# Kernel optimization log

Measured on AMD Instinct MI355X. Metric: run time of the kernel, lower is better.

The kernel has to match this reference:

```python
import jax, jax.numpy as jnp
import numpy as np

B, CY, CS, D, H, W = 4, 256, 256, 256, 64, 64


def pe2d(C, H, W, dtype=jnp.float32):
    """PositionalEncodingPermute2D: returns [C, H, W]. Assumes ch_half even (C=256 -> 128)."""
    ch_half = (C + 1) // 2
    inv = 1.0 / (10000.0 ** (jnp.arange(0, ch_half, 2, dtype=jnp.float32) / ch_half))  # [ch_half//2]
    tH = jnp.arange(H, dtype=jnp.float32)
    tW = jnp.arange(W, dtype=jnp.float32)
    sH = tH[:, None] * inv[None, :]                      # [H, ch_half//2]
    sW = tW[:, None] * inv[None, :]                      # [W, ch_half//2]
    embH = jnp.concatenate([jnp.sin(sH), jnp.cos(sH)], -1)  # [H, ch_half]
    embW = jnp.concatenate([jnp.sin(sW), jnp.cos(sW)], -1)  # [W, ch_half]
    E = jnp.zeros((H, W, 2 * ch_half), dtype=dtype)
    E = E.at[:, :, :ch_half].set(jnp.broadcast_to(embW[None, :, :], (H, W, ch_half)).astype(dtype))
    E = E.at[:, :, ch_half:2 * ch_half].set(jnp.broadcast_to(embH[:, None, :], (H, W, ch_half)).astype(dtype))
    return jnp.transpose(E[..., :C], (2, 0, 1))          # [C, H, W]


def conv1x1(x, w, b):
    # x: [B,Cin,H,W], w: [Cout,Cin], b: [Cout]
    return jnp.einsum('bchw,dc->bdhw', x, w) + b[None, :, None, None]


def setup_inputs() -> dict:
    key = jax.random.key(0)
    ks = jax.random.split(key, 12)
    s_in = 1.0 / np.sqrt(D)
    return {
        'Y': jax.random.normal(ks[0], (B, CY, H, W), jnp.float32),
        'S': jax.random.normal(ks[1], (B, CS, H, W), jnp.float32),
        'Wq': jax.random.normal(ks[2], (D, CY), jnp.float32) * s_in,
        'bq': jax.random.normal(ks[3], (D,), jnp.float32) * 0.01,
        'Wk': jax.random.normal(ks[4], (D, CS), jnp.float32) * s_in,
        'bk': jax.random.normal(ks[5], (D,), jnp.float32) * 0.01,
        'Wv': jax.random.normal(ks[6], (D, CS), jnp.float32) * s_in,
        'bv': jax.random.normal(ks[7], (D,), jnp.float32) * 0.01,
        'Wo': jax.random.normal(ks[8], (CS, D), jnp.float32) * s_in,
        'bo': jax.random.normal(ks[9], (CS,), jnp.float32) * 0.01,
    }


def reference(Y, S, Wq, bq, Wk, bk, Wv, bv, Wo, bo):
    b, _, h, w = Y.shape
    d = Wq.shape[0]
    scale = d ** (-0.5)
    Q = conv1x1(Y, Wq, bq)
    K = conv1x1(S, Wk, bk)
    V = conv1x1(S, Wv, bv)
    pe = pe2d(d, h, w, Q.dtype)[None]                    # [1,d,H,W]
    Q = Q + pe
    K = K + pe
    # flatten spatial -> [B, N, d]
    Qf = Q.reshape(b, d, h * w).transpose(0, 2, 1)
    Kf = K.reshape(b, d, h * w).transpose(0, 2, 1)
    Vf = V.reshape(b, d, h * w).transpose(0, 2, 1)
    A = jax.nn.softmax(jnp.einsum('bnd,bmd->bnm', Qf, Kf) * scale, axis=-1)
    Z = jnp.einsum('bnm,bmd->bnd', A, Vf)                # [B,N,d]
    Z = Z.transpose(0, 2, 1).reshape(b, d, h, w)
    return conv1x1(Z, Wo, bo)
```

## Files before the change

kernel.cpp:

```cpp
#include <hip/hip_runtime.h>
#include <stdint.h>


#define NB 4
#define CC 256
#define DD 256
#define NN 4096
#define PS (NB * NN * DD)

typedef float f32x4 __attribute__((ext_vector_type(4)));
typedef unsigned int u32x4 __attribute__((ext_vector_type(4)));
typedef unsigned int u32x2 __attribute__((ext_vector_type(2)));
typedef _Float16 f16x8 __attribute__((ext_vector_type(8)));
typedef __fp16 fp16x2 __attribute__((ext_vector_type(2)));

#define MFMAH(a, b, c) __builtin_amdgcn_mfma_f32_16x16x32_f16((a), (b), (c), 0, 0, 0)

__device__ __forceinline__ uint16_t h2u(_Float16 h) {
    return __builtin_bit_cast(unsigned short, h);
}
__device__ __forceinline__ uint32_t packh(_Float16 a, _Float16 b) {
    return (uint32_t)h2u(a) | ((uint32_t)h2u(b) << 16);
}
__device__ __forceinline__ f16x8 ldsh8(const void* p) {
    return __builtin_bit_cast(f16x8, *(const u32x4*)p);
}
__device__ __forceinline__ void split8h(const float* v, f16x8& hi, f16x8& lo) {
#pragma unroll
    for (int j = 0; j < 8; ++j) {
        _Float16 h = (_Float16)v[j];
        hi[j] = h;
        lo[j] = (_Float16)(v[j] - (float)h);
    }
}

__global__ __launch_bounds__(256) void proj_kernel(
    const float* __restrict__ Y, const float* __restrict__ S,
    const float* __restrict__ Wq, const float* __restrict__ bq,
    const float* __restrict__ Wk, const float* __restrict__ bk,
    const float* __restrict__ Wv, const float* __restrict__ bv,
    uint16_t* __restrict__ Qp, uint16_t* __restrict__ Kp,
    uint16_t* __restrict__ Vp) {
    __shared__ char XsH[64 * 64];
    __shared__ char XsL[64 * 64];
    __shared__ float Bz[64 * 68];

    int bi = blockIdx.x;
    int proj = bi >> 10;
    int rem = bi & 1023;
    int b = rem >> 8;
    int dt = (rem >> 6) & 3;
    int nt = rem & 63;
    int d0 = dt * 64, n0 = nt * 64;

    int t = threadIdx.x;
    int lane = t & 63, wv = t >> 6;
    int g = lane >> 4, li = lane & 15;

    const float* X = (proj == 0 ? Y : S) + (size_t)b * CC * NN;
    const float* W = proj == 0 ? Wq : (proj == 1 ? Wk : Wv);
    const float* bias = proj == 0 ? bq : (proj == 1 ? bk : bv);

    f32x4 acc[4];
#pragma unroll
    for (int i = 0; i < 4; ++i) acc[i] = (f32x4){0.f, 0.f, 0.f, 0.f};

    int nloc = t & 63;
    int cq = t >> 6;
    uint32_t spch = (uint32_t)(cq ^ ((nloc >> 1) & 3));
    uint32_t rpch = (uint32_t)(g ^ ((li >> 1) & 3));

    for (int kk = 0; kk < 8; ++kk) {
        int c0 = kk * 32;
        {
            const float* xp = X + (size_t)(c0 + cq * 8) * NN + n0 + nloc;
            float xv[8];
#pragma unroll
            for (int j = 0; j < 8; ++j) xv[j] = xp[(size_t)j * NN];
            u32x4 hw, lw;
#pragma unroll
            for (int w = 0; w < 4; ++w) {
                float x = xv[2 * w], y = xv[2 * w + 1];
                _Float16 hx = (_Float16)x, hy = (_Float16)y;
                hw[w] = packh(hx, hy);
                lw[w] = packh((_Float16)(x - (float)hx), (_Float16)(y - (float)hy));
            }
            *(u32x4*)(XsH + nloc * 64 + spch * 16) = hw;
            *(u32x4*)(XsL + nloc * 64 + spch * 16) = lw;
        }
        __syncthreads();
        const float* wr = W + (size_t)(d0 + wv * 16 + li) * CC + c0 + g * 8;
        float wvv[8];
        *(float4*)&wvv[0] = ((const float4*)wr)[0];
        *(float4*)&wvv[4] = ((const float4*)wr)[1];
        f16x8 wh, wl;
        split8h(wvv, wh, wl);
#pragma unroll
        for (int nf = 0; nf < 4; ++nf) {
            const char* bp = XsH + (nf * 16 + li) * 64 + rpch * 16;
            f16x8 xh = ldsh8(bp);
            f16x8 xl = ldsh8(XsL + (nf * 16 + li) * 64 + rpch * 16);
            acc[nf] = MFMAH(wh, xh, acc[nf]);
            acc[nf] = MFMAH(wh, xl, acc[nf]);
            acc[nf] = MFMAH(wl, xh, acc[nf]);
        }
        __syncthreads();
    }

    if (proj == 2) {
#pragma unroll
        for (int r = 0; r < 4; ++r) {
            int d = d0 + wv * 16 + g * 4 + r;
            float bs = bias[d];
#pragma unroll
            for (int nf = 0; nf < 4; ++nf) {
                int n = n0 + nf * 16 + li;
                float v = acc[nf][r] + bs;
                Vp[(size_t)(b * DD + d) * NN + n] = h2u((_Float16)v);
            }
        }
    } else {
        const float QSCALE = 0.0625f * 1.4426950408889634f;
#pragma unroll
        for (int r = 0; r < 4; ++r) {
            int d = d0 + wv * 16 + g * 4 + r;
            float bs = bias[d];
            int jj = d & 63;
            float inv = exp2f((float)jj * -0.20762050593046f);
#pragma unroll
            for (int nf = 0; nf < 4; ++nf) {
                int n = n0 + nf * 16 + li;
                float v = acc[nf][r] + bs;
                float pos = (d < 128) ? (float)(n & 63) : (float)(n >> 6);
                float ar = pos * inv;
                v += (d & 64) ? cosf(ar) : sinf(ar);
                if (proj == 0) v *= QSCALE;
                Bz[(nf * 16 + li) * 68 + wv * 16 + g * 4 + r] = v;
            }
        }
        __syncthreads();
        {
            int nl = t >> 2;
            int dk = (t & 3) * 16;
            float vv[16];
#pragma unroll
            for (int q = 0; q < 4; ++q)
                *(float4*)&vv[q * 4] = *(const float4*)&Bz[nl * 68 + dk + q * 4];
            u32x4 w0, w1;
#pragma unroll
            for (int w = 0; w < 4; ++w)
                w0[w] = packh((_Float16)vv[2 * w], (_Float16)vv[2 * w + 1]);
#pragma unroll
            for (int w = 0; w < 4; ++w)
                w1[w] = packh((_Float16)vv[8 + 2 * w], (_Float16)vv[9 + 2 * w]);
            uint16_t* Ph = (proj == 0) ? Qp : Kp;
            size_t o = (size_t)(b * NN + n0 + nl) * DD + d0 + dk;
            ((u32x4*)(Ph + o))[0] = w0;
            ((u32x4*)(Ph + o))[1] = w1;
        }
    }
}

__global__ __launch_bounds__(256, 1) void attn_kernel(
    const uint16_t* __restrict__ Qp, const uint16_t* __restrict__ Kp,
    const uint16_t* __restrict__ Vp,
    const float* __restrict__ Wo, const float* __restrict__ bo,
    float* __restrict__ Out) {
    extern __shared__ char smem[];

    int t = threadIdx.x;
    int lane = t & 63, wv = t >> 6;
    int g = lane >> 4, li = lane & 15;

    int orig = ((blockIdx.x & 7) << 5) + (blockIdx.x >> 3);
    int b = orig >> 6;
    int nt = orig & 63;
    int n0 = nt * 64;

    f16x8 qh[8];
    {
        size_t qrow = (size_t)(b * NN + n0 + wv * 16 + li) * DD;
#pragma unroll
        for (int kf = 0; kf < 8; ++kf)
            qh[kf] =
                __builtin_bit_cast(f16x8, *(const u32x4*)(Qp + qrow + kf * 32 + g * 8));
    }

    const uint16_t* splane;
    uint32_t dstbase, adv;
    uint32_t soff[16];
    if (wv < 2) {
        splane = Kp + (size_t)b * NN * DD;
        dstbase = (uint32_t)wv * 16384u;
        adv = 64 * 256;
#pragma unroll
        for (int i = 0; i < 16; ++i) {
            int rr = wv * 32 + 2 * i + (lane >> 5);
            int cc = lane & 31;
            soff[i] = (uint32_t)(rr * 256 + ((cc ^ (rr & 7)) * 8));
        }
    } else {
        splane = Vp + (size_t)b * DD * NN;
        dstbase = 65536u + (uint32_t)(wv - 2) * 16384u;
        adv = 64;
#pragma unroll
        for (int i = 0; i < 16; ++i) {
            int rr = (wv - 2) * 128 + i * 8 + (lane >> 3);
            int cc = lane & 7;
            soff[i] = (uint32_t)rr * 4096u + (uint32_t)((cc ^ (rr & 7)) * 8);
        }
    }

    uint32_t PB = 131072u + (uint32_t)wv * 2048u;
    uint32_t ka[8];
#pragma unroll
    for (int kf = 0; kf < 8; ++kf)
        ka[kf] = (uint32_t)li * 512u + (uint32_t)(((kf * 4 + g) ^ (li & 7)) * 16);
    uint32_t va0 = 65536u + (uint32_t)li * 128u + (uint32_t)(((g) ^ (li & 7)) * 16);
    uint32_t va1 = 65536u + (uint32_t)li * 128u + (uint32_t)(((4 + g) ^ (li & 7)) * 16);
    uint32_t pw[4];
#pragma unroll
    for (int mf = 0; mf < 4; ++mf)
        pw[mf] = PB + (uint32_t)li * 128u +
                 (uint32_t)((((2 * mf + (g >> 1))) ^ (li & 7)) * 16) +
                 (uint32_t)((g & 1) * 8);
    uint32_t pr0 = PB + (uint32_t)li * 128u + (uint32_t)(((g) ^ (li & 7)) * 16);
    uint32_t pr1 = PB + (uint32_t)li * 128u + (uint32_t)(((4 + g) ^ (li & 7)) * 16);

    f32x4 acc[16];
#pragma unroll
    for (int i = 0; i < 16; ++i) acc[i] = (f32x4){0.f, 0.f, 0.f, 0.f};
    float mrun = -__builtin_inff();
    float lrun = 0.f;
    f32x4 stA[4], stB[4];

#define STAGEX(tt)                                                                      \
    do {                                                                                \
        uint32_t mo = (uint32_t)(tt)*adv;                                               \
        char* db = smem + (uint32_t)(((tt)&1) * 32768u) + dstbase;                      \
        _Pragma("unroll") for (int i = 0; i < 16; ++i) {                                \
            __builtin_amdgcn_global_load_lds(                                           \
                (const __attribute__((address_space(1))) unsigned int*)(splane +        \
                                                                        soff[i] + mo),  \
                (__attribute__((address_space(3))) unsigned int*)(db + i * 1024), 16, 0,\
                0);                                                                     \
        }                                                                               \
    } while (0)

#define QKPART(T, SC)                                                                   \
    {                                                                                   \
        _Pragma("unroll") for (int mf = 0; mf < 4; ++mf) SC[mf] =                       \
            (f32x4){0.f, 0.f, 0.f, 0.f};                                                \
        __builtin_amdgcn_s_setprio(1);                                                  \
        _Pragma("unroll") for (int kf = 0; kf < 8; ++kf) {                              \
            _Pragma("unroll") for (int mf = 0; mf < 4; ++mf) {                          \
                f16x8 kfr = ldsh8(smem + ka[kf] +                                       \
                                  (uint32_t)(((T)&1) * 32768u + mf * 8192u));           \
                SC[mf] = MFMAH(kfr, qh[kf], SC[mf]);                                    \
            }                                                                           \
        }                                                                               \
        __builtin_amdgcn_s_setprio(0);                                                  \
    }

#define SMPV(T, SP)                                                                     \
    {                                                                                   \
        float sv[16];                                                                   \
        _Pragma("unroll") for (int mf = 0; mf < 4; ++mf)                                \
            _Pragma("unroll") for (int r = 0; r < 4; ++r) sv[mf * 4 + r] = SP[mf][r];   \
        float pm = sv[0];                                                               \
        _Pragma("unroll") for (int j = 1; j < 16; ++j) pm = fmaxf(pm, sv[j]);           \
        pm = fmaxf(pm, __shfl_xor(pm, 16));                                             \
        pm = fmaxf(pm, __shfl_xor(pm, 32));                                             \
        if (__any(pm > mrun + 5.77f)) {                                                 \
            float mnew = fmaxf(mrun, pm);                                               \
            float fac = exp2f(mrun - mnew);                                             \
            lrun *= fac;                                                                \
            _Pragma("unroll") for (int i2 = 0; i2 < 16; ++i2) {                         \
                acc[i2][0] *= fac; acc[i2][1] *= fac;                                   \
                acc[i2][2] *= fac; acc[i2][3] *= fac;                                   \
            }                                                                           \
            mrun = mnew;                                                                \
        }                                                                               \
        float p[16];                                                                    \
        float ps = 0.f;                                                                 \
        _Pragma("unroll") for (int j = 0; j < 16; ++j) {                                \
            p[j] = exp2f(sv[j] - mrun);                                                 \
            ps += p[j];                                                                 \
        }                                                                               \
        uint32_t hw[8];                                                                 \
        _Pragma("unroll") for (int w = 0; w < 8; ++w) hw[w] = __builtin_bit_cast(       \
            uint32_t, __builtin_amdgcn_cvt_pkrtz(p[2 * w], p[2 * w + 1]));              \
        _Pragma("unroll") for (int mf = 0; mf < 4; ++mf) {                              \
            *(u32x2*)(smem + pw[mf]) = (u32x2){hw[2 * mf], hw[2 * mf + 1]};             \
        }                                                                               \
        ps += __shfl_xor(ps, 16);                                                       \
        ps += __shfl_xor(ps, 32);                                                       \
        lrun += ps;                                                                     \
        f16x8 pbh0 = ldsh8(smem + pr0);                                                 \
        f16x8 pbh1 = ldsh8(smem + pr1);                                                 \
        __builtin_amdgcn_s_setprio(1);                                                  \
        _Pragma("unroll") for (int df = 0; df < 16; ++df) {                             \
            uint32_t vo = (uint32_t)((((T)&1) ? 0u : 32768u) + df * 2048u);             \
            f16x8 v0 = ldsh8(smem + va0 + vo);                                          \
            f16x8 v1 = ldsh8(smem + va1 + vo);                                          \
            acc[df] = MFMAH(v0, pbh0, acc[df]);                                         \
            acc[df] = MFMAH(v1, pbh1, acc[df]);                                         \
        }                                                                               \
        __builtin_amdgcn_s_setprio(0);                                                  \
    }

#define ITER(T, SC, SP, DOSM, VMC)                                                      \
    {                                                                                   \
        asm volatile("s_waitcnt vmcnt(" #VMC ")" ::: "memory");                         \
        __builtin_amdgcn_s_barrier();                                                   \
        QKPART(T, SC);                                                                  \
        if (DOSM) SMPV(T, SP);                                                          \
        asm volatile("s_waitcnt lgkmcnt(0)" ::: "memory");                              \
        __builtin_amdgcn_s_barrier();                                                   \
        if (((T) < 62) && (wv < 2)) STAGEX((T) + 2);                                    \
        if (((T) < 63) && (wv >= 2)) STAGEX((T) + 1);                                   \
    }

    if (wv < 2) {
        STAGEX(0);
        STAGEX(1);
    } else {
        STAGEX(0);
    }

    ITER(0, stA, stB, 0, 16);
#pragma unroll 1
    for (int tp = 0; tp < 31; ++tp) {
        ITER(2 * tp + 1, stB, stA, 1, 16);
        ITER(2 * tp + 2, stA, stB, 1, 16);
    }
    ITER(63, stB, stA, 1, 0);
    SMPV(64, stB);

#undef ITER
#undef SMPV
#undef QKPART
#undef STAGEX

    float rl = 1.0f / lrun;
    char* zh = smem;
    char* zl = smem + 32768;
    {
        int n = wv * 16 + li;
#pragma unroll
        for (int df = 0; df < 16; ++df) {
#pragma unroll
            for (int rp = 0; rp < 2; ++rp) {
                float a0 = acc[df][2 * rp] * rl, a1 = acc[df][2 * rp + 1] * rl;
                _Float16 h0 = (_Float16)a0, h1 = (_Float16)a1;
                uint32_t whi = packh(h0, h1);
                uint32_t wlo =
                    packh((_Float16)(a0 - (float)h0), (_Float16)(a1 - (float)h1));
                uint32_t chunk = (uint32_t)((df * 2 + (g >> 1)) ^ (li & 7));
                uint32_t off = (uint32_t)n * 512 + chunk * 16 + (g & 1) * 8 + rp * 4;
                *(uint32_t*)(zh + off) = whi;
                *(uint32_t*)(zl + off) = wlo;
            }
        }
    }
    __syncthreads();

    f32x4 oc[4][4];
#pragma unroll
    for (int i = 0; i < 4; ++i)
#pragma unroll
        for (int j = 0; j < 4; ++j) oc[i][j] = (f32x4){0.f, 0.f, 0.f, 0.f};
    int cs0 = wv * 64;
#pragma unroll 1
    for (int kf = 0; kf < 8; ++kf) {
        f16x8 zhv[4], zlv[4];
#pragma unroll
        for (int nf = 0; nf < 4; ++nf) {
            uint32_t off = (uint32_t)(nf * 16 + li) * 512 +
                           (uint32_t)((kf * 4 + g) ^ (li & 7)) * 16;
            zhv[nf] = ldsh8(zh + off);
            zlv[nf] = ldsh8(zl + off);
        }
#pragma unroll
        for (int csf = 0; csf < 4; ++csf) {
            const float* wr = Wo + (size_t)(cs0 + csf * 16 + li) * DD + kf * 32 + g * 8;
            float wvv[8];
            *(float4*)&wvv[0] = ((const float4*)wr)[0];
            *(float4*)&wvv[4] = ((const float4*)wr)[1];
            f16x8 wh, wl;
            split8h(wvv, wh, wl);
#pragma unroll
            for (int nf = 0; nf < 4; ++nf) {
                oc[csf][nf] = MFMAH(wh, zhv[nf], oc[csf][nf]);
                oc[csf][nf] = MFMAH(wh, zlv[nf], oc[csf][nf]);
                oc[csf][nf] = MFMAH(wl, zhv[nf], oc[csf][nf]);
            }
        }
    }
#pragma unroll
    for (int csf = 0; csf < 4; ++csf) {
#pragma unroll
        for (int r = 0; r < 4; ++r) {
            int cs = cs0 + csf * 16 + g * 4 + r;
            float bb = bo[cs];
#pragma unroll
            for (int nf = 0; nf < 4; ++nf)
                Out[(size_t)(b * 256 + cs) * NN + n0 + nf * 16 + li] =
                    oc[csf][nf][r] + bb;
        }
    }
}

extern "C" void kernel_launch(void* const* d_in, const int* in_sizes, int n_in,
                              void* d_out, int out_size, void* d_ws, size_t ws_size,
                              hipStream_t stream) {
    (void)in_sizes; (void)n_in; (void)out_size; (void)ws_size;
    const float* Y = (const float*)d_in[0];
    const float* S = (const float*)d_in[1];
    const float* Wq = (const float*)d_in[2];
    const float* bq = (const float*)d_in[3];
    const float* Wk = (const float*)d_in[4];
    const float* bk = (const float*)d_in[5];
    const float* Wv = (const float*)d_in[6];
    const float* bv = (const float*)d_in[7];
    const float* Wo = (const float*)d_in[8];
    const float* bo = (const float*)d_in[9];
    float* Out = (float*)d_out;

    uint16_t* ws = (uint16_t*)d_ws;
    uint16_t* Qp = ws + 0 * (size_t)PS;
    uint16_t* Kp = ws + 1 * (size_t)PS;
    uint16_t* Vp = ws + 2 * (size_t)PS;

    (void)hipFuncSetAttribute((const void*)attn_kernel,
                              hipFuncAttributeMaxDynamicSharedMemorySize, 139264);

    proj_kernel<<<3072, 256, 0, stream>>>(Y, S, Wq, bq, Wk, bk, Wv, bv, Qp, Kp, Vp);
    attn_kernel<<<256, 256, 139264, stream>>>(Qp, Kp, Vp, Wo, bo, Out);
}
```

Baseline: 302.8 us.

## Split each key tile across two wave groups and merge softmax partials

```diff
diff --git a/kernel.cpp b/kernel.cpp
--- a/kernel.cpp
+++ b/kernel.cpp
@@ -161,7 +161,7 @@
     }
 }
 
-__global__ __launch_bounds__(256, 1) void attn_kernel(
+__global__ __launch_bounds__(512, 2) void attn_kernel(
     const uint16_t* __restrict__ Qp, const uint16_t* __restrict__ Kp,
     const uint16_t* __restrict__ Vp,
     const float* __restrict__ Wo, const float* __restrict__ bo,
@@ -171,6 +171,7 @@
     int t = threadIdx.x;
     int lane = t & 63, wv = t >> 6;
     int g = lane >> 4, li = lane & 15;
+    int qf = wv & 3, h = wv >> 2;
 
     int orig = ((blockIdx.x & 7) << 5) + (blockIdx.x >> 3);
     int b = orig >> 6;
@@ -179,7 +180,7 @@
 
     f16x8 qh[8];
     {
-        size_t qrow = (size_t)(b * NN + n0 + wv * 16 + li) * DD;
+        size_t qrow = (size_t)(b * NN + n0 + qf * 16 + li) * DD;
 #pragma unroll
         for (int kf = 0; kf < 8; ++kf)
             qh[kf] =
@@ -188,24 +189,24 @@
 
     const uint16_t* splane;
     uint32_t dstbase, adv;
-    uint32_t soff[16];
-    if (wv < 2) {
+    uint32_t soff[8];
+    if (wv < 4) {
         splane = Kp + (size_t)b * NN * DD;
-        dstbase = (uint32_t)wv * 16384u;
+        dstbase = (uint32_t)wv * 8192u;
         adv = 64 * 256;
 #pragma unroll
-        for (int i = 0; i < 16; ++i) {
-            int rr = wv * 32 + 2 * i + (lane >> 5);
+        for (int i = 0; i < 8; ++i) {
+            int rr = wv * 16 + 2 * i + (lane >> 5);
             int cc = lane & 31;
             soff[i] = (uint32_t)(rr * 256 + ((cc ^ (rr & 7)) * 8));
         }
     } else {
         splane = Vp + (size_t)b * DD * NN;
-        dstbase = 65536u + (uint32_t)(wv - 2) * 16384u;
+        dstbase = 65536u + (uint32_t)(wv - 4) * 8192u;
         adv = 64;
 #pragma unroll
-        for (int i = 0; i < 16; ++i) {
-            int rr = (wv - 2) * 128 + i * 8 + (lane >> 3);
+        for (int i = 0; i < 8; ++i) {
+            int rr = (wv - 4) * 64 + i * 8 + (lane >> 3);
             int cc = lane & 7;
             soff[i] = (uint32_t)rr * 4096u + (uint32_t)((cc ^ (rr & 7)) * 8);
         }
@@ -215,30 +216,30 @@
     uint32_t ka[8];
 #pragma unroll
     for (int kf = 0; kf < 8; ++kf)
-        ka[kf] = (uint32_t)li * 512u + (uint32_t)(((kf * 4 + g) ^ (li & 7)) * 16);
-    uint32_t va0 = 65536u + (uint32_t)li * 128u + (uint32_t)(((g) ^ (li & 7)) * 16);
-    uint32_t va1 = 65536u + (uint32_t)li * 128u + (uint32_t)(((4 + g) ^ (li & 7)) * 16);
-    uint32_t pw[4];
-#pragma unroll
-    for (int mf = 0; mf < 4; ++mf)
+        ka[kf] = (uint32_t)(h * 32 + li) * 512u +
+                 (uint32_t)(((kf * 4 + g) ^ (li & 7)) * 16);
+    uint32_t va = 65536u + (uint32_t)li * 128u +
+                  (uint32_t)(((h * 4 + g) ^ (li & 7)) * 16);
+    uint32_t pw[2];
+#pragma unroll
+    for (int mf = 0; mf < 2; ++mf)
         pw[mf] = PB + (uint32_t)li * 128u +
-                 (uint32_t)((((2 * mf + (g >> 1))) ^ (li & 7)) * 16) +
+                 (uint32_t)((((mf * 2 + (g >> 1))) ^ (li & 7)) * 16) +
                  (uint32_t)((g & 1) * 8);
-    uint32_t pr0 = PB + (uint32_t)li * 128u + (uint32_t)(((g) ^ (li & 7)) * 16);
-    uint32_t pr1 = PB + (uint32_t)li * 128u + (uint32_t)(((4 + g) ^ (li & 7)) * 16);
+    uint32_t pr = PB + (uint32_t)li * 128u + (uint32_t)((g ^ (li & 7)) * 16);
 
     f32x4 acc[16];
 #pragma unroll
     for (int i = 0; i < 16; ++i) acc[i] = (f32x4){0.f, 0.f, 0.f, 0.f};
     float mrun = -__builtin_inff();
     float lrun = 0.f;
-    f32x4 stA[4], stB[4];
+    f32x4 stA[2], stB[2];
 
 #define STAGEX(tt)                                                                      \
     do {                                                                                \
         uint32_t mo = (uint32_t)(tt)*adv;                                               \
         char* db = smem + (uint32_t)(((tt)&1) * 32768u) + dstbase;                      \
-        _Pragma("unroll") for (int i = 0; i < 16; ++i) {                                \
+        _Pragma("unroll") for (int i = 0; i < 8; ++i) {                                 \
             __builtin_amdgcn_global_load_lds(                                           \
                 (const __attribute__((address_space(1))) unsigned int*)(splane +        \
                                                                         soff[i] + mo),  \
@@ -249,11 +250,11 @@
 
 #define QKPART(T, SC)                                                                   \
     {                                                                                   \
-        _Pragma("unroll") for (int mf = 0; mf < 4; ++mf) SC[mf] =                       \
+        _Pragma("unroll") for (int mf = 0; mf < 2; ++mf) SC[mf] =                       \
             (f32x4){0.f, 0.f, 0.f, 0.f};                                                \
         __builtin_amdgcn_s_setprio(1);                                                  \
         _Pragma("unroll") for (int kf = 0; kf < 8; ++kf) {                              \
-            _Pragma("unroll") for (int mf = 0; mf < 4; ++mf) {                          \
+            _Pragma("unroll") for (int mf = 0; mf < 2; ++mf) {                          \
                 f16x8 kfr = ldsh8(smem + ka[kf] +                                       \
                                   (uint32_t)(((T)&1) * 32768u + mf * 8192u));           \
                 SC[mf] = MFMAH(kfr, qh[kf], SC[mf]);                                    \
@@ -264,11 +265,11 @@
 
 #define SMPV(T, SP)                                                                     \
     {                                                                                   \
-        float sv[16];                                                                   \
-        _Pragma("unroll") for (int mf = 0; mf < 4; ++mf)                                \
+        float sv[8];                                                                    \
+        _Pragma("unroll") for (int mf = 0; mf < 2; ++mf)                                \
             _Pragma("unroll") for (int r = 0; r < 4; ++r) sv[mf * 4 + r] = SP[mf][r];   \
         float pm = sv[0];                                                               \
-        _Pragma("unroll") for (int j = 1; j < 16; ++j) pm = fmaxf(pm, sv[j]);           \
+        _Pragma("unroll") for (int j = 1; j < 8; ++j) pm = fmaxf(pm, sv[j]);            \
         pm = fmaxf(pm, __shfl_xor(pm, 16));                                             \
         pm = fmaxf(pm, __shfl_xor(pm, 32));                                             \
         if (__any(pm > mrun + 5.77f)) {                                                 \
@@ -281,30 +282,27 @@
             }                                                                           \
             mrun = mnew;                                                                \
         }                                                                               \
-        float p[16];                                                                    \
+        float p[8];                                                                     \
         float ps = 0.f;                                                                 \
-        _Pragma("unroll") for (int j = 0; j < 16; ++j) {                                \
+        _Pragma("unroll") for (int j = 0; j < 8; ++j) {                                 \
             p[j] = exp2f(sv[j] - mrun);                                                 \
             ps += p[j];                                                                 \
         }                                                                               \
-        uint32_t hw[8];                                                                 \
-        _Pragma("unroll") for (int w = 0; w < 8; ++w) hw[w] = __builtin_bit_cast(       \
+        uint32_t hw[4];                                                                 \
+        _Pragma("unroll") for (int w = 0; w < 4; ++w) hw[w] = __builtin_bit_cast(       \
             uint32_t, __builtin_amdgcn_cvt_pkrtz(p[2 * w], p[2 * w + 1]));              \
-        _Pragma("unroll") for (int mf = 0; mf < 4; ++mf) {                              \
+        _Pragma("unroll") for (int mf = 0; mf < 2; ++mf) {                              \
             *(u32x2*)(smem + pw[mf]) = (u32x2){hw[2 * mf], hw[2 * mf + 1]};             \
         }                                                                               \
         ps += __shfl_xor(ps, 16);                                                       \
         ps += __shfl_xor(ps, 32);                                                       \
         lrun += ps;                                                                     \
-        f16x8 pbh0 = ldsh8(smem + pr0);                                                 \
-        f16x8 pbh1 = ldsh8(smem + pr1);                                                 \
+        f16x8 pb = ldsh8(smem + pr);                                                    \
         __builtin_amdgcn_s_setprio(1);                                                  \
         _Pragma("unroll") for (int df = 0; df < 16; ++df) {                             \
             uint32_t vo = (uint32_t)((((T)&1) ? 0u : 32768u) + df * 2048u);             \
-            f16x8 v0 = ldsh8(smem + va0 + vo);                                          \
-            f16x8 v1 = ldsh8(smem + va1 + vo);                                          \
-            acc[df] = MFMAH(v0, pbh0, acc[df]);                                         \
-            acc[df] = MFMAH(v1, pbh1, acc[df]);                                         \
+            f16x8 v0 = ldsh8(smem + va + vo);                                           \
+            acc[df] = MFMAH(v0, pb, acc[df]);                                           \
         }                                                                               \
         __builtin_amdgcn_s_setprio(0);                                                  \
     }
@@ -317,22 +315,22 @@
         if (DOSM) SMPV(T, SP);                                                          \
         asm volatile("s_waitcnt lgkmcnt(0)" ::: "memory");                              \
         __builtin_amdgcn_s_barrier();                                                   \
-        if (((T) < 62) && (wv < 2)) STAGEX((T) + 2);                                    \
-        if (((T) < 63) && (wv >= 2)) STAGEX((T) + 1);                                   \
-    }
-
-    if (wv < 2) {
+        if (((T) < 62) && (wv < 4)) STAGEX((T) + 2);                                    \
+        if (((T) < 63) && (wv >= 4)) STAGEX((T) + 1);                                   \
+    }
+
+    if (wv < 4) {
         STAGEX(0);
         STAGEX(1);
     } else {
         STAGEX(0);
     }
 
-    ITER(0, stA, stB, 0, 16);
+    ITER(0, stA, stB, 0, 8);
 #pragma unroll 1
     for (int tp = 0; tp < 31; ++tp) {
-        ITER(2 * tp + 1, stB, stA, 1, 16);
-        ITER(2 * tp + 2, stA, stB, 1, 16);
+        ITER(2 * tp + 1, stB, stA, 1, 8);
+        ITER(2 * tp + 2, stA, stB, 1, 8);
     }
     ITER(63, stB, stA, 1, 0);
     SMPV(64, stB);
@@ -342,11 +340,41 @@
 #undef QKPART
 #undef STAGEX
 
-    float rl = 1.0f / lrun;
-    char* zh = smem;
-    char* zl = smem + 32768;
-    {
-        int n = wv * 16 + li;
+    __syncthreads();
+    if (wv >= 4) {
+        uint32_t wb = 65536u + (uint32_t)(wv - 4) * 16384u;
+#pragma unroll
+        for (int df = 0; df < 16; ++df)
+            *(f32x4*)(smem + wb + (uint32_t)df * 1024u + (uint32_t)lane * 16u) =
+                acc[df];
+        *(float*)(smem + 147456u + (uint32_t)(wv - 4) * 512u + (uint32_t)lane * 8u) =
+            mrun;
+        *(float*)(smem + 147456u + (uint32_t)(wv - 4) * 512u + (uint32_t)lane * 8u +
+                  4u) = lrun;
+    }
+    __syncthreads();
+
+    if (wv < 4) {
+        float m2 =
+            *(const float*)(smem + 147456u + (uint32_t)wv * 512u + (uint32_t)lane * 8u);
+        float l2 = *(const float*)(smem + 147456u + (uint32_t)wv * 512u +
+                                   (uint32_t)lane * 8u + 4u);
+        float mN = fmaxf(mrun, m2);
+        float f1 = exp2f(mrun - mN);
+        float f2 = exp2f(m2 - mN);
+        float lm = lrun * f1 + l2 * f2;
+        uint32_t wb = 65536u + (uint32_t)wv * 16384u;
+#pragma unroll
+        for (int df = 0; df < 16; ++df) {
+            f32x4 a2 =
+                *(const f32x4*)(smem + wb + (uint32_t)df * 1024u + (uint32_t)lane * 16u);
+#pragma unroll
+            for (int r = 0; r < 4; ++r) acc[df][r] = acc[df][r] * f1 + a2[r] * f2;
+        }
+        float rl = 1.0f / lm;
+        char* zh = smem;
+        char* zl = smem + 32768;
+        int n = qf * 16 + li;
 #pragma unroll
         for (int df = 0; df < 16; ++df) {
 #pragma unroll
@@ -365,12 +393,14 @@
     }
     __syncthreads();
 
-    f32x4 oc[4][4];
-#pragma unroll
-    for (int i = 0; i < 4; ++i)
+    const char* zh = smem;
+    const char* zl = smem + 32768;
+    f32x4 oc[2][4];
+#pragma unroll
+    for (int i = 0; i < 2; ++i)
 #pragma unroll
         for (int j = 0; j < 4; ++j) oc[i][j] = (f32x4){0.f, 0.f, 0.f, 0.f};
-    int cs0 = wv * 64;
+    int cs0 = wv * 32;
 #pragma unroll 1
     for (int kf = 0; kf < 8; ++kf) {
         f16x8 zhv[4], zlv[4];
@@ -382,7 +412,7 @@
             zlv[nf] = ldsh8(zl + off);
         }
 #pragma unroll
-        for (int csf = 0; csf < 4; ++csf) {
+        for (int csf = 0; csf < 2; ++csf) {
             const float* wr = Wo + (size_t)(cs0 + csf * 16 + li) * DD + kf * 32 + g * 8;
             float wvv[8];
             *(float4*)&wvv[0] = ((const float4*)wr)[0];
@@ -398,7 +428,7 @@
         }
     }
 #pragma unroll
-    for (int csf = 0; csf < 4; ++csf) {
+    for (int csf = 0; csf < 2; ++csf) {
 #pragma unroll
         for (int r = 0; r < 4; ++r) {
             int cs = cs0 + csf * 16 + g * 4 + r;
@@ -433,8 +463,8 @@
     uint16_t* Vp = ws + 2 * (size_t)PS;
 
     (void)hipFuncSetAttribute((const void*)attn_kernel,
-                              hipFuncAttributeMaxDynamicSharedMemorySize, 139264);
+                              hipFuncAttributeMaxDynamicSharedMemorySize, 149504);
 
     proj_kernel<<<3072, 256, 0, stream>>>(Y, S, Wq, bq, Wk, bk, Wv, bv, Qp, Kp, Vp);
-    attn_kernel<<<256, 256, 139264, stream>>>(Qp, Kp, Vp, Wo, bo, Out);
-}
+    attn_kernel<<<256, 512, 149504, stream>>>(Qp, Kp, Vp, Wo, bo, Out);
+}
```

Result: faster. 259.1 us (-14.4%).
